# Kernel tuning notes

Measured on AMD Instinct MI355X. Metric: run time of the kernel, lower is better.

Reference implementation:

```python
import jax, jax.numpy as jnp
import numpy as np

B, W, KD, NC, D, NN, NH, AD, HOPS = 512, 4, 64, 32, 256, 16, 8, 32, 4
DH = D // NH
DFF = 4 * D
P = B * W + B
ROLE_WRITER, ROLE_QUERY = 0, 1


def setup_inputs() -> dict:
    key = jax.random.key(0)
    ks = iter(jax.random.split(key, 40))
    f = lambda shape, s=0.02: jax.random.normal(next(ks), shape, dtype=jnp.float32) * s
    inp = {
        'query_keys': jax.random.normal(next(ks), (B, KD), dtype=jnp.float32),
        'writer_keys': jax.random.normal(next(ks), (B, W, KD), dtype=jnp.float32),
        'key_proj_w': f((KD, D)), 'key_proj_b': jnp.zeros((D,), jnp.float32),
        'class_embed': f((NC, D)), 'role_embed': f((3, D)), 'start_node_embed': f((NN, D)),
        'input_ln_g': jnp.ones((D,), jnp.float32), 'input_ln_b': jnp.zeros((D,), jnp.float32),
        'ln1_g': jnp.ones((NN, D), jnp.float32), 'ln1_b': jnp.zeros((NN, D), jnp.float32),
        'wqkv': f((NN, D, 3 * D)), 'bqkv': jnp.zeros((NN, 3 * D), jnp.float32),
        'wo': f((NN, D, D)), 'bo': jnp.zeros((NN, D), jnp.float32),
        'ln2_g': jnp.ones((NN, D), jnp.float32), 'ln2_b': jnp.zeros((NN, D), jnp.float32),
        'w_fc1': f((NN, D, DFF)), 'b_fc1': jnp.zeros((NN, DFF), jnp.float32),
        'w_fc2': f((NN, DFF, D)), 'b_fc2': jnp.zeros((NN, D), jnp.float32),
        'delta_w': jnp.zeros((D, D), jnp.float32), 'delta_b': jnp.zeros((D,), jnp.float32),
        'dir_w': f((D, D)), 'dir_b': jnp.zeros((D,), jnp.float32),
        'mag_w': f((D, 1)), 'mag_b': jnp.full((1,), 2.5, jnp.float32),
        'out_w': f((D, NC)), 'out_b': jnp.zeros((NC,), jnp.float32),
        'address_table': jax.random.normal(next(ks), (NN, AD), dtype=jnp.float32),
        'query_start_nodes': jax.random.randint(next(ks), (B,), 0, NN),
        'writer_labels': jax.random.randint(next(ks), (B, W), 0, NC),
        'writer_start_nodes': jax.random.randint(next(ks), (B, W), 0, NN),
    }
    return inp


def _ln(x):
    m = jnp.mean(x, -1, keepdims=True)
    v = jnp.var(x, -1, keepdims=True)
    return (x - m) * jax.lax.rsqrt(v + 1e-5)


def _forward(query_keys, writer_keys, key_proj_w, key_proj_b, class_embed, role_embed,
             start_node_embed, input_ln_g, input_ln_b, ln1_g, ln1_b, wqkv, bqkv, wo, bo,
             ln2_g, ln2_b, w_fc1, b_fc1, w_fc2, b_fc2, delta_w, delta_b, dir_w, dir_b,
             mag_w, mag_b, out_w, out_b, address_table,
             query_start_nodes, writer_labels, writer_start_nodes):
    # ---- encode writers (encode_writers) ----
    fk = writer_keys.reshape(-1, KD)          # [B*W, KD]
    fl = writer_labels.reshape(-1)            # [B*W]
    fs = writer_start_nodes.reshape(-1)       # [B*W]
    learned_w = fk @ key_proj_w + key_proj_b + class_embed[fl] + start_node_embed[fs] + role_embed[ROLE_WRITER]
    sw = jnp.zeros_like(learned_w).at[:, :KD].set(fk)
    sw = sw.at[:, KD:KD + NC].set(jax.nn.one_hot(fl, NC, dtype=learned_w.dtype))
    enc_w = _ln(learned_w) * input_ln_g + input_ln_b + sw
    # ---- encode queries (encode_queries) ----
    learned_q = query_keys @ key_proj_w + key_proj_b + start_node_embed[query_start_nodes] + role_embed[ROLE_QUERY]
    sq = jnp.zeros_like(learned_q).at[:, :KD].set(query_keys)
    enc_q = _ln(learned_q) * input_ln_g + input_ln_b + sq

    h = jnp.concatenate([enc_w, enc_q], axis=0)          # [P, D]
    node = jnp.concatenate([fs, query_start_nodes], 0)   # [P] current compute node per packet

    inv_sqrt_dh = 1.0 / np.sqrt(DH).astype(np.float32)
    for _ in range(HOPS):
        oh = jax.nn.one_hot(node, NN, dtype=h.dtype)      # [P, NN] dispatch weights

        def pnl(x, Wn, bn):
            # per-node linear: gather-compute-scatter via MoE-style dense dispatch
            xe = jnp.einsum('pn,pd->npd', oh, x)          # [NN, P, din]
            ye = jnp.einsum('npd,ndf->npf', xe, Wn)       # [NN, P, dout]
            return jnp.einsum('npf,pn->pf', ye, oh) + oh @ bn

        # ComputeNodeCell: pre-LN attention among packets at the same node
        x = _ln(h) * (oh @ ln1_g) + oh @ ln1_b
        qkv = pnl(x, wqkv, bqkv)                          # [P, 3D]
        q, k, v = jnp.split(qkv, 3, axis=-1)
        q = q.reshape(P, NH, DH); k = k.reshape(P, NH, DH); v = v.reshape(P, NH, DH)
        scores = jnp.einsum('phd,qhd->hpq', q, k) * inv_sqrt_dh   # [NH, P, P]
        same = node[:, None] == node[None, :]
        scores = jnp.where(same[None], scores, -1e9)
        attn = jax.nn.softmax(scores, axis=-1)
        ao = jnp.einsum('hpq,qhd->phd', attn, v).reshape(P, D)
        h = h + pnl(ao, wo, bo)
        # MLP block
        x2 = _ln(h) * (oh @ ln2_g) + oh @ ln2_b
        h = h + pnl(jax.nn.gelu(pnl(x2, w_fc1, b_fc1)), w_fc2, b_fc2)
        # routing heads: pick next node from address table, apply gated delta
        direction = h @ dir_w + dir_b
        node = jnp.argmax(direction[:, :AD] @ address_table.T, axis=-1)
        h = h + (h @ delta_w + delta_b) * jax.nn.sigmoid(h @ mag_w + mag_b)

    return h @ out_w + out_b                              # [P, NC] per-packet logits


def reference(query_keys, writer_keys, key_proj_w, key_proj_b, class_embed, role_embed,
              start_node_embed, input_ln_g, input_ln_b, ln1_g, ln1_b, wqkv, bqkv, wo, bo,
              ln2_g, ln2_b, w_fc1, b_fc1, w_fc2, b_fc2, delta_w, delta_b, dir_w, dir_b,
              mag_w, mag_b, out_w, out_b, address_table,
              query_start_nodes, writer_labels, writer_start_nodes):
    return _forward(query_keys, writer_keys, key_proj_w, key_proj_b, class_embed, role_embed,
                    start_node_embed, input_ln_g, input_ln_b, ln1_g, ln1_b, wqkv, bqkv, wo, bo,
                    ln2_g, ln2_b, w_fc1, b_fc1, w_fc2, b_fc2, delta_w, delta_b, dir_w, dir_b,
                    mag_w, mag_b, out_w, out_b, address_table,
                    query_start_nodes, writer_labels, writer_start_nodes)
```

## Files before the change

kernel.cpp:

```cpp
#include <hip/hip_runtime.h>
#include <math.h>

#define B_    512
#define W_    4
#define KD_   64
#define NC_   32
#define D_    256
#define NN_   16
#define NH_   8
#define AD_   32
#define HOPS_ 4
#define DH_   32
#define DFF_  1024
#define P_    2560
#define BW_   2048
#define MAXT_ 56

#define INV_SQRT_DH 0.17677669529663687f

__device__ __forceinline__ float block_sum256(float v, float* red) {
#pragma unroll
  for (int off = 32; off > 0; off >>= 1) v += __shfl_xor(v, off, 64);
  int wid = threadIdx.x >> 6;
  if ((threadIdx.x & 63) == 0) red[wid] = v;
  __syncthreads();
  float s = red[0] + red[1] + red[2] + red[3];
  __syncthreads();
  return s;
}

__device__ __forceinline__ float gelu_tanh(float v) {
  float u = 0.7978845608028654f * (v + 0.044715f * v * v * v);
  return 0.5f * v * (1.0f + tanhf(u));
}

__global__ __launch_bounds__(256) void encode_kernel(
    const float* __restrict__ query_keys, const float* __restrict__ writer_keys,
    const float* __restrict__ kpw, const float* __restrict__ kpb,
    const float* __restrict__ ce, const float* __restrict__ re,
    const float* __restrict__ sne, const float* __restrict__ ilg,
    const float* __restrict__ ilb, const int* __restrict__ qsn,
    const int* __restrict__ wl, const int* __restrict__ wsn,
    float* __restrict__ h, int* __restrict__ node) {
  int p = blockIdx.x, t = threadIdx.x;
  __shared__ float fk[KD_];
  __shared__ float red[4];
  const float* key;
  int lab = -1, sn, role;
  if (p < BW_) { key = writer_keys + (size_t)p * KD_; lab = wl[p]; sn = wsn[p]; role = 0; }
  else { int b = p - BW_; key = query_keys + (size_t)b * KD_; sn = qsn[b]; role = 1; }
  if (t < KD_) fk[t] = key[t];
  __syncthreads();

  float acc = kpb[t] + sne[sn * D_ + t] + re[role * D_ + t];
  if (lab >= 0) acc += ce[lab * D_ + t];
#pragma unroll 8
  for (int i = 0; i < KD_; i++) acc += fk[i] * kpw[i * D_ + t];

  float mean = block_sum256(acc, red) * (1.0f / D_);
  float d = acc - mean;
  float var = block_sum256(d * d, red) * (1.0f / D_);
  float xn = d * (1.0f / sqrtf(var + 1e-5f));

  float sw = 0.0f;
  if (t < KD_) sw = fk[t];
  else if (lab >= 0 && t < KD_ + NC_) sw = (t - KD_ == lab) ? 1.0f : 0.0f;

  h[(size_t)p * D_ + t] = xn * ilg[t] + ilb[t] + sw;
  if (t == 0) node[p] = sn;
}

__global__ __launch_bounds__(256) void sort_kernel(const int* __restrict__ node,
                                                   int* __restrict__ order,
                                                   int* __restrict__ invord,
                                                   int* __restrict__ offs,
                                                   int* __restrict__ cnts,
                                                   int* __restrict__ tnode,
                                                   int* __restrict__ tstart,
                                                   int* __restrict__ tend,
                                                   int* __restrict__ ntiles) {
  __shared__ int c[NN_], o[NN_], cur[NN_];
  int t = threadIdx.x;
  if (t < NN_) c[t] = 0;
  __syncthreads();
  for (int p = t; p < P_; p += 256) atomicAdd(&c[node[p]], 1);
  __syncthreads();
  if (t == 0) {
    int s = 0;
    for (int n = 0; n < NN_; n++) { o[n] = s; cur[n] = s; s += c[n]; }
    int idx = 0;
    for (int n = 0; n < NN_; n++) {
      int e = o[n] + c[n];
      for (int m0 = o[n]; m0 < e; m0 += 64) {
        tnode[idx] = n; tstart[idx] = m0; tend[idx] = e; idx++;
      }
    }
    ntiles[0] = idx;
  }
  __syncthreads();
  if (t < NN_) { cnts[t] = c[t]; offs[t] = o[t]; }
  for (int p = t; p < P_; p += 256) {
    int r = atomicAdd(&cur[node[p]], 1);
    order[r] = p;
    invord[p] = r;
  }
}

__global__ __launch_bounds__(256) void ln_affine(const float* __restrict__ h,
                                                 const float* __restrict__ g,
                                                 const float* __restrict__ b,
                                                 const int* __restrict__ node,
                                                 const int* __restrict__ order,
                                                 float* __restrict__ x) {
  int sp = blockIdx.x * 4 + (threadIdx.x >> 6);
  int lane = threadIdx.x & 63;
  int p = order[sp];
  int n = node[p];
  float4 v = *(const float4*)&h[(size_t)p * D_ + lane * 4];
  float s = v.x + v.y + v.z + v.w;
#pragma unroll
  for (int off = 32; off > 0; off >>= 1) s += __shfl_xor(s, off, 64);
  float mean = s * (1.0f / D_);
  float4 d = make_float4(v.x - mean, v.y - mean, v.z - mean, v.w - mean);
  float vr = d.x * d.x + d.y * d.y + d.z * d.z + d.w * d.w;
#pragma unroll
  for (int off = 32; off > 0; off >>= 1) vr += __shfl_xor(vr, off, 64);
  float inv = 1.0f / sqrtf(vr * (1.0f / D_) + 1e-5f);
  float4 gg = *(const float4*)&g[n * D_ + lane * 4];
  float4 bb = *(const float4*)&b[n * D_ + lane * 4];
  float4 o;
  o.x = d.x * inv * gg.x + bb.x;
  o.y = d.y * inv * gg.y + bb.y;
  o.z = d.z * inv * gg.z + bb.z;
  o.w = d.w * inv * gg.w + bb.w;
  *(float4*)&x[(size_t)sp * D_ + lane * 4] = o;
}

template <int DIN, int DOUT, int JT, int ACT, int RESID, int PER_NODE, int KSPLIT, int XMODE>
__global__ __launch_bounds__(256) void glin(const float* __restrict__ x,
                                            const float* __restrict__ W,
                                            const float* __restrict__ bias,
                                            float* __restrict__ out,
                                            float* __restrict__ pbuf,
                                            const float* __restrict__ xaux,
                                            const int* __restrict__ order,
                                            const int* __restrict__ invord,
                                            const int* __restrict__ tnode,
                                            const int* __restrict__ tstart,
                                            const int* __restrict__ tend,
                                            const int* __restrict__ ntiles) {
  constexpr int KC = 32, STX = 68;
  constexpr int CPT = JT / 16;
  constexpr int HALF = 64;
  constexpr int KLEN = DIN / KSPLIT;
  constexpr int NCH = KLEN / KC;
  constexpr int LPR = JT / 4;
  constexpr int RPI = 64 / LPR;

  int ti = blockIdx.x;
  int n, s0, s1;
  if (PER_NODE) {
    if (ti >= ntiles[0]) return;
    n = tnode[ti]; s0 = tstart[ti]; s1 = tend[ti];
  } else {
    n = 0; s0 = ti * 64; s1 = P_;
  }
  int jbase = blockIdx.y * JT;
  int kz = (KSPLIT > 1) ? blockIdx.z : 0;
  int k0 = kz * KLEN;
  int rows = s1 - s0; if (rows > 64) rows = 64;

  __shared__ float xs[2][KC][STX];
  __shared__ float ws[2][KC][JT];

  int tid = threadIdx.x;
  const float* Wn = W + (size_t)n * DIN * DOUT + jbase;

  int xrow = tid >> 2, xq = tid & 3;
  bool xvalid = xrow < rows;
  const float* xptr = x + (size_t)(s0 + (xvalid ? xrow : 0)) * DIN + k0 + xq * 4;
  const float* aptr = nullptr;
  if (XMODE == 1) {
    int pr = xvalid ? invord[s0 + xrow] : 0;
    aptr = xaux + (size_t)pr * DIN + k0 + xq * 4;
  }

  float4 xr0, xr1;
  auto xfetch = [&](int kc) {
    if (xvalid) {
      xr0 = *(const float4*)(xptr + kc);
      xr1 = *(const float4*)(xptr + kc + 16);
      if (XMODE == 1) {
        float4 p0 = *(const float4*)(aptr + kc);
        float4 p1 = *(const float4*)(aptr + kc + 16);
        xr0.x += p0.x; xr0.y += p0.y; xr0.z += p0.z; xr0.w += p0.w;
        xr1.x += p1.x; xr1.y += p1.y; xr1.z += p1.z; xr1.w += p1.w;
      }
    } else {
      xr0 = make_float4(0.f, 0.f, 0.f, 0.f);
      xr1 = make_float4(0.f, 0.f, 0.f, 0.f);
    }
  };
  auto xstage = [&](int buf) {
    xs[buf][xq * 4 + 0][xrow] = xr0.x;
    xs[buf][xq * 4 + 1][xrow] = xr0.y;
    xs[buf][xq * 4 + 2][xrow] = xr0.z;
    xs[buf][xq * 4 + 3][xrow] = xr0.w;
    xs[buf][xq * 4 + 16][xrow] = xr1.x;
    xs[buf][xq * 4 + 17][xrow] = xr1.y;
    xs[buf][xq * 4 + 18][xrow] = xr1.z;
    xs[buf][xq * 4 + 19][xrow] = xr1.w;
  };
  int wvw = tid >> 6, lane = tid & 63;
  int wlr = lane / LPR;
  int wlc = (lane % LPR) * 4;
  auto wfetch = [&](int buf, int kc) {
#pragma unroll
    for (int i = 0; i < 8 / RPI; i++) {
      int kr = wvw * 8 + i * RPI;
      const float* g = &Wn[(size_t)(k0 + kc + kr + wlr) * DOUT + wlc];
      __builtin_amdgcn_global_load_lds(
          (const __attribute__((address_space(1))) unsigned int*)g,
          (__attribute__((address_space(3))) unsigned int*)&ws[buf][kr][0],
          16, 0, 0);
    }
  };

  wfetch(0, 0);
  xfetch(0);
  xstage(0);
  __syncthreads();

  int r4 = (tid >> 4) * 4;
  int jc4 = (tid & 15) * 4;
  float acc[4][CPT];
#pragma unroll
  for (int r = 0; r < 4; r++)
#pragma unroll
    for (int cc = 0; cc < CPT; cc++) acc[r][cc] = 0.f;

  for (int c = 0; c < NCH; c++) {
    int cur = c & 1;
    if (c + 1 < NCH) {
      wfetch(cur ^ 1, (c + 1) * KC);
      xfetch((c + 1) * KC);
    }
#pragma unroll 8
    for (int k = 0; k < KC; k++) {
      float4 a = *(const float4*)&xs[cur][k][r4];
      float av[4] = {a.x, a.y, a.z, a.w};
      float bv[CPT];
      float4 b0 = *(const float4*)&ws[cur][k][jc4];
      bv[0] = b0.x; bv[1] = b0.y; bv[2] = b0.z; bv[3] = b0.w;
      if (CPT == 8) {
        float4 b1 = *(const float4*)&ws[cur][k][jc4 + HALF];
        bv[4] = b1.x; bv[5] = b1.y; bv[6] = b1.z; bv[7] = b1.w;
      }
#pragma unroll
      for (int r = 0; r < 4; r++)
#pragma unroll
        for (int cc = 0; cc < CPT; cc++) acc[r][cc] += av[r] * bv[cc];
    }
    if (c + 1 < NCH) xstage(cur ^ 1);
    __syncthreads();
  }

  bool main_part = (KSPLIT == 1) || (kz == 0);
  float bbv[CPT];
#pragma unroll
  for (int cc = 0; cc < 4; cc++) bbv[cc] = bias[n * DOUT + jbase + jc4 + cc];
  if (CPT == 8) {
#pragma unroll
    for (int cc = 0; cc < 4; cc++) bbv[4 + cc] = bias[n * DOUT + jbase + jc4 + HALF + cc];
  }

#pragma unroll
  for (int r = 0; r < 4; r++) {
    int lr = r4 + r;
    if (lr >= rows) continue;
    float v[CPT];
    if (main_part) {
#pragma unroll
      for (int cc = 0; cc < CPT; cc++) {
        v[cc] = acc[r][cc] + bbv[cc];
        if (ACT == 1) v[cc] = gelu_tanh(v[cc]);
      }
      if (RESID) {
        int pp = PER_NODE ? order[s0 + lr] : (s0 + lr);
        float* op = &out[(size_t)pp * DOUT + jbase + jc4];
        {
          float4 old = *(const float4*)op;
          *(float4*)op = make_float4(v[0] + old.x, v[1] + old.y, v[2] + old.z, v[3] + old.w);
        }
        if (CPT == 8) {
          float4 old = *(const float4*)(op + HALF);
          *(float4*)(op + HALF) =
              make_float4(v[4] + old.x, v[5] + old.y, v[6] + old.z, v[7] + old.w);
        }
      } else {
        float* op = &out[(size_t)(s0 + lr) * DOUT + jbase + jc4];
        *(float4*)op = make_float4(v[0], v[1], v[2], v[3]);
        if (CPT == 8)
          *(float4*)(op + HALF) = make_float4(v[4], v[5], v[6], v[7]);
      }
    } else {
      float* op = &pbuf[(size_t)(s0 + lr) * DOUT + jbase + jc4];
      *(float4*)op = make_float4(acc[r][0], acc[r][1], acc[r][2], acc[r][3]);
      if (CPT == 8)
        *(float4*)(op + HALF) = make_float4(acc[r][4], acc[r][5], acc[r][6], acc[r][7]);
    }
  }
}

#define ATS 36
__global__ __launch_bounds__(256) void attn_kernel(const float* __restrict__ qkv,
                                                   const int* __restrict__ node,
                                                   const int* __restrict__ order,
                                                   const int* __restrict__ offs,
                                                   const int* __restrict__ cnts,
                                                   float* __restrict__ ao) {
  __shared__ float qs[32 * ATS];
  __shared__ float kts[32 * ATS];
  __shared__ float vs[32 * ATS];
  __shared__ float ps[32 * ATS];
  __shared__ int glo[32], ghi[32];

  int t = threadIdx.x;
  int r = t >> 3;
  int j4 = (t & 7) * 4;
  int r0 = blockIdx.x * 32;
  int hd = blockIdx.y;

  if (t < 32) {
    int n = node[order[r0 + t]];
    glo[t] = offs[n];
    ghi[t] = offs[n] + cnts[n];
  }
  __syncthreads();

  {
    const float* qp = &qkv[(size_t)(r0 + r) * 768 + hd * 32 + j4];
    float4 q4 = *(const float4*)qp;
    q4.x *= INV_SQRT_DH; q4.y *= INV_SQRT_DH; q4.z *= INV_SQRT_DH; q4.w *= INV_SQRT_DH;
    *(float4*)&qs[r * ATS + j4] = q4;
  }

  int lo = glo[0];
  int hi = ghi[31];
  int myglo = glo[r], myghi = ghi[r];

  float4 o4 = {0.f, 0.f, 0.f, 0.f};
  float mrow = -1e30f, lrow = 0.f;

  for (int kt = lo; kt < hi; kt += 32) {
    int sj = kt + r;
    float4 k4 = {0.f, 0.f, 0.f, 0.f}, v4 = {0.f, 0.f, 0.f, 0.f};
    if (sj < hi) {
      const float* kp = &qkv[(size_t)sj * 768 + 256 + hd * 32 + j4];
      k4 = *(const float4*)kp;
      v4 = *(const float4*)(kp + 256);
    }
    __syncthreads();
    kts[(j4 + 0) * ATS + r] = k4.x;
    kts[(j4 + 1) * ATS + r] = k4.y;
    kts[(j4 + 2) * ATS + r] = k4.z;
    kts[(j4 + 3) * ATS + r] = k4.w;
    *(float4*)&vs[r * ATS + j4] = v4;
    __syncthreads();

    float s0 = 0.f, s1 = 0.f, s2 = 0.f, s3 = 0.f;
#pragma unroll 8
    for (int d = 0; d < 32; d++) {
      float qv = qs[r * ATS + d];
      float4 kv = *(const float4*)&kts[d * ATS + j4];
      s0 += qv * kv.x; s1 += qv * kv.y; s2 += qv * kv.z; s3 += qv * kv.w;
    }
    int c0 = kt + j4;
    if (c0 + 0 < myglo || c0 + 0 >= myghi) s0 = -1e30f;
    if (c0 + 1 < myglo || c0 + 1 >= myghi) s1 = -1e30f;
    if (c0 + 2 < myglo || c0 + 2 >= myghi) s2 = -1e30f;
    if (c0 + 3 < myglo || c0 + 3 >= myghi) s3 = -1e30f;

    float mx = fmaxf(fmaxf(s0, s1), fmaxf(s2, s3));
#pragma unroll
    for (int off = 4; off > 0; off >>= 1) mx = fmaxf(mx, __shfl_xor(mx, off, 8));
    float mnew = fmaxf(mrow, mx);
    float alpha = __expf(mrow - mnew);
    float p0 = __expf(s0 - mnew), p1 = __expf(s1 - mnew);
    float p2 = __expf(s2 - mnew), p3 = __expf(s3 - mnew);
    float ls = p0 + p1 + p2 + p3;
#pragma unroll
    for (int off = 4; off > 0; off >>= 1) ls += __shfl_xor(ls, off, 8);
    lrow = lrow * alpha + ls;
    mrow = mnew;
    o4.x *= alpha; o4.y *= alpha; o4.z *= alpha; o4.w *= alpha;

    *(float4*)&ps[r * ATS + j4] = make_float4(p0, p1, p2, p3);
#pragma unroll 8
    for (int j = 0; j < 32; j++) {
      float pj = ps[r * ATS + j];
      float4 vv = *(const float4*)&vs[j * ATS + j4];
      o4.x += pj * vv.x; o4.y += pj * vv.y; o4.z += pj * vv.z; o4.w += pj * vv.w;
    }
  }

  float inv = 1.f / lrow;
  o4.x *= inv; o4.y *= inv; o4.z *= inv; o4.w *= inv;
  *(float4*)&ao[(size_t)(r0 + r) * D_ + hd * 32 + j4] = o4;
}

__global__ __launch_bounds__(256) void route_kernel(float* __restrict__ h,
                                                    const float* __restrict__ pbuf,
                                                    const int* __restrict__ invord,
                                                    const float* __restrict__ dir_w,
                                                    const float* __restrict__ dir_b,
                                                    const float* __restrict__ at,
                                                    const float* __restrict__ mag_w,
                                                    const float* __restrict__ mag_b,
                                                    const float* __restrict__ delta,
                                                    int* __restrict__ node) {
  int p = blockIdx.x, t = threadIdx.x;
  __shared__ float hs[D_];
  __shared__ float dpart[8][AD_];
  __shared__ float dirs[AD_];
  __shared__ float scs[NN_];
  __shared__ float red[4];
  float hv = h[(size_t)p * D_ + t] + pbuf[(size_t)invord[p] * D_ + t];
  hs[t] = hv;
  __syncthreads();

  int j = t & 31, seg = t >> 5;
  float part = 0.0f;
#pragma unroll 8
  for (int i = 0; i < 32; i++) {
    int ii = seg * 32 + i;
    part += hs[ii] * dir_w[ii * D_ + j];
  }
  dpart[seg][j] = part;
  __syncthreads();
  if (t < AD_) {
    float s = dir_b[t];
#pragma unroll
    for (int g = 0; g < 8; g++) s += dpart[g][t];
    dirs[t] = s;
  }
  __syncthreads();
  if (t < NN_) {
    float s = 0.0f;
#pragma unroll
    for (int a = 0; a < AD_; a++) s += dirs[a] * at[t * AD_ + a];
    scs[t] = s;
  }
  __syncthreads();
  if (t == 0) {
    float best = scs[0];
    int arg = 0;
    for (int nn = 1; nn < NN_; nn++)
      if (scs[nn] > best) { best = scs[nn]; arg = nn; }
    node[p] = arg;
  }
  float mag = block_sum256(hv * mag_w[t], red) + mag_b[0];
  float sig = 1.0f / (1.0f + __expf(-mag));
  h[(size_t)p * D_ + t] = hv + delta[(size_t)p * D_ + t] * sig;
}

__global__ __launch_bounds__(256) void out_kernel(const float* __restrict__ h,
                                                  const float* __restrict__ ow,
                                                  const float* __restrict__ ob,
                                                  float* __restrict__ out) {
  int p = blockIdx.x, t = threadIdx.x;
  __shared__ float hs[D_];
  __shared__ float part[8][NC_];
  hs[t] = h[(size_t)p * D_ + t];
  __syncthreads();
  int j = t & 31, seg = t >> 5;
  float s = 0.0f;
#pragma unroll 8
  for (int i = 0; i < 32; i++) {
    int ii = seg * 32 + i;
    s += hs[ii] * ow[ii * NC_ + j];
  }
  part[seg][j] = s;
  __syncthreads();
  if (t < NC_) {
    float r = ob[t];
#pragma unroll
    for (int g = 0; g < 8; g++) r += part[g][t];
    out[(size_t)p * NC_ + t] = r;
  }
}

extern "C" void kernel_launch(void* const* d_in, const int* in_sizes, int n_in,
                              void* d_out, int out_size, void* d_ws, size_t ws_size,
                              hipStream_t stream) {
  (void)in_sizes; (void)n_in; (void)out_size; (void)ws_size;
  const float* query_keys       = (const float*)d_in[0];
  const float* writer_keys      = (const float*)d_in[1];
  const float* key_proj_w       = (const float*)d_in[2];
  const float* key_proj_b       = (const float*)d_in[3];
  const float* class_embed      = (const float*)d_in[4];
  const float* role_embed       = (const float*)d_in[5];
  const float* start_node_embed = (const float*)d_in[6];
  const float* input_ln_g       = (const float*)d_in[7];
  const float* input_ln_b       = (const float*)d_in[8];
  const float* ln1_g            = (const float*)d_in[9];
  const float* ln1_b            = (const float*)d_in[10];
  const float* wqkv             = (const float*)d_in[11];
  const float* bqkv             = (const float*)d_in[12];
  const float* wo               = (const float*)d_in[13];
  const float* bo               = (const float*)d_in[14];
  const float* ln2_g            = (const float*)d_in[15];
  const float* ln2_b            = (const float*)d_in[16];
  const float* w_fc1            = (const float*)d_in[17];
  const float* b_fc1            = (const float*)d_in[18];
  const float* w_fc2            = (const float*)d_in[19];
  const float* b_fc2            = (const float*)d_in[20];
  const float* delta_w          = (const float*)d_in[21];
  const float* delta_b          = (const float*)d_in[22];
  const float* dir_w            = (const float*)d_in[23];
  const float* dir_b            = (const float*)d_in[24];
  const float* mag_w            = (const float*)d_in[25];
  const float* mag_b            = (const float*)d_in[26];
  const float* out_w            = (const float*)d_in[27];
  const float* out_b            = (const float*)d_in[28];
  const float* address_table    = (const float*)d_in[29];
  const int* query_start_nodes  = (const int*)d_in[30];
  const int* writer_labels      = (const int*)d_in[31];
  const int* writer_start_nodes = (const int*)d_in[32];

  uintptr_t basep = (uintptr_t)d_ws;
  auto carve = [&](size_t bytes) {
    basep = (basep + 255) & ~(uintptr_t)255;
    void* r = (void*)basep;
    basep += bytes;
    return r;
  };
  float* h    = (float*)carve((size_t)P_ * D_ * 4);
  float* x    = (float*)carve((size_t)P_ * D_ * 4);
  float* buf1 = (float*)carve((size_t)P_ * DFF_ * 4);
  float* ff   = (float*)carve((size_t)P_ * DFF_ * 4);
  float* pbuf = (float*)carve((size_t)P_ * D_ * 4);
  int* node   = (int*)carve(P_ * 4);
  int* order  = (int*)carve(P_ * 4);
  int* invord = (int*)carve(P_ * 4);
  int* offs   = (int*)carve(NN_ * 4);
  int* cnts   = (int*)carve(NN_ * 4);
  int* tnode  = (int*)carve(MAXT_ * 4);
  int* tstart = (int*)carve(MAXT_ * 4);
  int* tend   = (int*)carve(MAXT_ * 4);
  int* ntiles = (int*)carve(4);

  encode_kernel<<<P_, 256, 0, stream>>>(query_keys, writer_keys, key_proj_w, key_proj_b,
                                        class_embed, role_embed, start_node_embed,
                                        input_ln_g, input_ln_b, query_start_nodes,
                                        writer_labels, writer_start_nodes, h, node);

  for (int hop = 0; hop < HOPS_; ++hop) {
    sort_kernel<<<1, 256, 0, stream>>>(node, order, invord, offs, cnts,
                                       tnode, tstart, tend, ntiles);
    ln_affine<<<P_ / 4, 256, 0, stream>>>(h, ln1_g, ln1_b, node, order, x);
    glin<256, 768, 64, 0, 0, 1, 1, 0><<<dim3(MAXT_, 12), 256, 0, stream>>>(
        x, wqkv, bqkv, buf1, nullptr, nullptr, order, invord, tnode, tstart, tend,
        ntiles);
    attn_kernel<<<dim3(P_ / 32, NH_), 256, 0, stream>>>(buf1, node, order, offs,
                                                        cnts, x );
    glin<256, 256, 64, 0, 1, 1, 1, 0><<<dim3(MAXT_, 4), 256, 0, stream>>>(
        x, wo, bo, h, nullptr, nullptr, order, invord, tnode, tstart, tend, ntiles);
    ln_affine<<<P_ / 4, 256, 0, stream>>>(h, ln2_g, ln2_b, node, order, x);
    glin<256, 1024, 64, 1, 0, 1, 1, 0><<<dim3(MAXT_, 16), 256, 0, stream>>>(
        x, w_fc1, b_fc1, ff, nullptr, nullptr, order, invord, tnode, tstart, tend,
        ntiles);
    glin<1024, 256, 64, 0, 1, 1, 2, 0><<<dim3(MAXT_, 4, 2), 256, 0, stream>>>(
        ff, w_fc2, b_fc2, h, pbuf, nullptr, order, invord, tnode, tstart, tend,
        ntiles);
    glin<256, 256, 64, 0, 0, 0, 1, 1><<<dim3(P_ / 64, 4), 256, 0, stream>>>(
        h, delta_w, delta_b, buf1 , nullptr, pbuf, order, invord,
        tnode, tstart, tend, ntiles);
    route_kernel<<<P_, 256, 0, stream>>>(h, pbuf, invord, dir_w, dir_b, address_table,
                                         mag_w, mag_b, buf1, node);
  }

  out_kernel<<<P_, 256, 0, stream>>>(h, out_w, out_b, (float*)d_out);
}
```

Baseline: 910.1 us.

## Replace LDS-tiled grouped GEMM with register-streamed 16-row tiles and XCD swizzle

Replaces the shared-memory double-buffered GEMM with a kernel that streams weights straight from global memory into registers. Each wave handles 4 rows of a 16-row tile and each thread owns 4 output columns across a 256-wide column block. The sort kernel now emits 16-row tiles per node, which cuts padding waste for small node groups. Block indices are also swizzled across XCDs. In exchange, each weight is reused by fewer rows, so weight traffic through L2 rises, and activation buffers are padded so tail tiles can read past the last row safely.

```diff
diff --git a/kernel.cpp b/kernel.cpp
--- a/kernel.cpp
+++ b/kernel.cpp
@@ -14,7 +14,7 @@
 #define DFF_  1024
 #define P_    2560
 #define BW_   2048
-#define MAXT_ 56
+#define MAXT2_ 176
 
 #define INV_SQRT_DH 0.17677669529663687f
 
@@ -91,7 +91,7 @@
     int idx = 0;
     for (int n = 0; n < NN_; n++) {
       int e = o[n] + c[n];
-      for (int m0 = o[n]; m0 < e; m0 += 64) {
+      for (int m0 = o[n]; m0 < e; m0 += 16) {
         tnode[idx] = n; tstart[idx] = m0; tend[idx] = e; idx++;
       }
     }
@@ -136,178 +136,151 @@
   *(float4*)&x[(size_t)sp * D_ + lane * 4] = o;
 }
 
-template <int DIN, int DOUT, int JT, int ACT, int RESID, int PER_NODE, int KSPLIT, int XMODE>
-__global__ __launch_bounds__(256) void glin(const float* __restrict__ x,
-                                            const float* __restrict__ W,
-                                            const float* __restrict__ bias,
-                                            float* __restrict__ out,
-                                            float* __restrict__ pbuf,
-                                            const float* __restrict__ xaux,
-                                            const int* __restrict__ order,
-                                            const int* __restrict__ invord,
-                                            const int* __restrict__ tnode,
-                                            const int* __restrict__ tstart,
-                                            const int* __restrict__ tend,
-                                            const int* __restrict__ ntiles) {
-  constexpr int KC = 32, STX = 68;
-  constexpr int CPT = JT / 16;
-  constexpr int HALF = 64;
+template <int DIN, int DOUT, int ACT, int RESID, int PER_NODE, int KSPLIT, int XMODE>
+__global__ __launch_bounds__(256) void glin2(const float* __restrict__ x,
+                                             const float* __restrict__ W,
+                                             const float* __restrict__ bias,
+                                             float* __restrict__ out,
+                                             float* __restrict__ pbuf,
+                                             const float* __restrict__ xaux,
+                                             const int* __restrict__ order,
+                                             const int* __restrict__ invord,
+                                             const int* __restrict__ tnode,
+                                             const int* __restrict__ tstart,
+                                             const int* __restrict__ tend,
+                                             const int* __restrict__ ntiles) {
   constexpr int KLEN = DIN / KSPLIT;
-  constexpr int NCH = KLEN / KC;
-  constexpr int LPR = JT / 4;
-  constexpr int RPI = 64 / LPR;
-
-  int ti = blockIdx.x;
-  int n, s0, s1;
+
+  int gx = gridDim.x;
+  int bid = blockIdx.x;
+  int ti = (bid & 7) * (gx >> 3) + (bid >> 3);
+
+  int n, s0, rows;
   if (PER_NODE) {
     if (ti >= ntiles[0]) return;
-    n = tnode[ti]; s0 = tstart[ti]; s1 = tend[ti];
+    n = tnode[ti];
+    s0 = tstart[ti];
+    int e = tend[ti];
+    rows = e - s0;
+    if (rows > 16) rows = 16;
   } else {
-    n = 0; s0 = ti * 64; s1 = P_;
-  }
-  int jbase = blockIdx.y * JT;
+    n = 0;
+    s0 = ti * 16;
+    rows = 16;
+  }
+  int jb = blockIdx.y * 256;
   int kz = (KSPLIT > 1) ? blockIdx.z : 0;
   int k0 = kz * KLEN;
-  int rows = s1 - s0; if (rows > 64) rows = 64;
-
-  __shared__ float xs[2][KC][STX];
-  __shared__ float ws[2][KC][JT];
 
   int tid = threadIdx.x;
-  const float* Wn = W + (size_t)n * DIN * DOUT + jbase;
-
-  int xrow = tid >> 2, xq = tid & 3;
-  bool xvalid = xrow < rows;
-  const float* xptr = x + (size_t)(s0 + (xvalid ? xrow : 0)) * DIN + k0 + xq * 4;
-  const float* aptr = nullptr;
-  if (XMODE == 1) {
-    int pr = xvalid ? invord[s0 + xrow] : 0;
-    aptr = xaux + (size_t)pr * DIN + k0 + xq * 4;
-  }
-
-  float4 xr0, xr1;
-  auto xfetch = [&](int kc) {
-    if (xvalid) {
-      xr0 = *(const float4*)(xptr + kc);
-      xr1 = *(const float4*)(xptr + kc + 16);
-      if (XMODE == 1) {
-        float4 p0 = *(const float4*)(aptr + kc);
-        float4 p1 = *(const float4*)(aptr + kc + 16);
-        xr0.x += p0.x; xr0.y += p0.y; xr0.z += p0.z; xr0.w += p0.w;
-        xr1.x += p1.x; xr1.y += p1.y; xr1.z += p1.z; xr1.w += p1.w;
-      }
-    } else {
-      xr0 = make_float4(0.f, 0.f, 0.f, 0.f);
-      xr1 = make_float4(0.f, 0.f, 0.f, 0.f);
-    }
-  };
-  auto xstage = [&](int buf) {
-    xs[buf][xq * 4 + 0][xrow] = xr0.x;
-    xs[buf][xq * 4 + 1][xrow] = xr0.y;
-    xs[buf][xq * 4 + 2][xrow] = xr0.z;
-    xs[buf][xq * 4 + 3][xrow] = xr0.w;
-    xs[buf][xq * 4 + 16][xrow] = xr1.x;
-    xs[buf][xq * 4 + 17][xrow] = xr1.y;
-    xs[buf][xq * 4 + 18][xrow] = xr1.z;
-    xs[buf][xq * 4 + 19][xrow] = xr1.w;
-  };
-  int wvw = tid >> 6, lane = tid & 63;
-  int wlr = lane / LPR;
-  int wlc = (lane % LPR) * 4;
-  auto wfetch = [&](int buf, int kc) {
-#pragma unroll
-    for (int i = 0; i < 8 / RPI; i++) {
-      int kr = wvw * 8 + i * RPI;
-      const float* g = &Wn[(size_t)(k0 + kc + kr + wlr) * DOUT + wlc];
-      __builtin_amdgcn_global_load_lds(
-          (const __attribute__((address_space(1))) unsigned int*)g,
-          (__attribute__((address_space(3))) unsigned int*)&ws[buf][kr][0],
-          16, 0, 0);
-    }
-  };
-
-  wfetch(0, 0);
-  xfetch(0);
-  xstage(0);
-  __syncthreads();
-
-  int r4 = (tid >> 4) * 4;
-  int jc4 = (tid & 15) * 4;
-  float acc[4][CPT];
-#pragma unroll
-  for (int r = 0; r < 4; r++)
-#pragma unroll
-    for (int cc = 0; cc < CPT; cc++) acc[r][cc] = 0.f;
-
-  for (int c = 0; c < NCH; c++) {
-    int cur = c & 1;
-    if (c + 1 < NCH) {
-      wfetch(cur ^ 1, (c + 1) * KC);
-      xfetch((c + 1) * KC);
-    }
-#pragma unroll 8
-    for (int k = 0; k < KC; k++) {
-      float4 a = *(const float4*)&xs[cur][k][r4];
-      float av[4] = {a.x, a.y, a.z, a.w};
-      float bv[CPT];
-      float4 b0 = *(const float4*)&ws[cur][k][jc4];
-      bv[0] = b0.x; bv[1] = b0.y; bv[2] = b0.z; bv[3] = b0.w;
-      if (CPT == 8) {
-        float4 b1 = *(const float4*)&ws[cur][k][jc4 + HALF];
-        bv[4] = b1.x; bv[5] = b1.y; bv[6] = b1.z; bv[7] = b1.w;
-      }
-#pragma unroll
-      for (int r = 0; r < 4; r++)
-#pragma unroll
-        for (int cc = 0; cc < CPT; cc++) acc[r][cc] += av[r] * bv[cc];
-    }
-    if (c + 1 < NCH) xstage(cur ^ 1);
-    __syncthreads();
-  }
-
+  int wv = __builtin_amdgcn_readfirstlane((int)(tid >> 6));
+  int j4 = (tid & 63) << 2;
+
+  const float* Wp = W + (size_t)n * DIN * DOUT + (size_t)k0 * DOUT + jb + j4;
+
+  const float* xr0;
+  const float* xr1;
+  const float* xr2;
+  const float* xr3;
+  const float* ar0 = nullptr;
+  const float* ar1 = nullptr;
+  const float* ar2 = nullptr;
+  const float* ar3 = nullptr;
+  {
+    int rbase = s0 + (wv << 2);
+    xr0 = x + (size_t)(rbase + 0) * DIN + k0;
+    xr1 = x + (size_t)(rbase + 1) * DIN + k0;
+    xr2 = x + (size_t)(rbase + 2) * DIN + k0;
+    xr3 = x + (size_t)(rbase + 3) * DIN + k0;
+    if (XMODE == 1) {
+      ar0 = xaux + (size_t)invord[rbase + 0] * DIN + k0;
+      ar1 = xaux + (size_t)invord[rbase + 1] * DIN + k0;
+      ar2 = xaux + (size_t)invord[rbase + 2] * DIN + k0;
+      ar3 = xaux + (size_t)invord[rbase + 3] * DIN + k0;
+    }
+  }
+
+  float4 a0 = make_float4(0.f, 0.f, 0.f, 0.f);
+  float4 a1 = a0, a2 = a0, a3 = a0;
+  float4 wc0, wc1, wc2, wc3, xc0, xc1, xc2, xc3;
+
+#define LDW_(kk, w0, w1, w2, w3)                              \
+  w0 = *(const float4*)(Wp + (size_t)((kk) + 0) * DOUT);      \
+  w1 = *(const float4*)(Wp + (size_t)((kk) + 1) * DOUT);      \
+  w2 = *(const float4*)(Wp + (size_t)((kk) + 2) * DOUT);      \
+  w3 = *(const float4*)(Wp + (size_t)((kk) + 3) * DOUT);
+
+#define LDX1_(kk, ptr, aptr, dst)                             \
+  dst = *(const float4*)((ptr) + (kk));                       \
+  if (XMODE == 1) {                                           \
+    float4 _a = *(const float4*)((aptr) + (kk));              \
+    dst.x += _a.x; dst.y += _a.y; dst.z += _a.z; dst.w += _a.w; \
+  }
+
+#define LDX_(kk, x0, x1, x2, x3)   \
+  LDX1_(kk, xr0, ar0, x0)          \
+  LDX1_(kk, xr1, ar1, x1)          \
+  LDX1_(kk, xr2, ar2, x2)          \
+  LDX1_(kk, xr3, ar3, x3)
+
+  LDW_(0, wc0, wc1, wc2, wc3);
+  LDX_(0, xc0, xc1, xc2, xc3);
+
+#pragma unroll 2
+  for (int kk = 0; kk < KLEN; kk += 4) {
+    float4 wn0, wn1, wn2, wn3, xn0, xn1, xn2, xn3;
+    bool more = (kk + 4 < KLEN);
+    if (more) {
+      LDW_(kk + 4, wn0, wn1, wn2, wn3);
+      LDX_(kk + 4, xn0, xn1, xn2, xn3);
+    }
+#pragma unroll
+    for (int t = 0; t < 4; ++t) {
+      float4 wt = (t == 0) ? wc0 : (t == 1) ? wc1 : (t == 2) ? wc2 : wc3;
+      float f0 = (t == 0) ? xc0.x : (t == 1) ? xc0.y : (t == 2) ? xc0.z : xc0.w;
+      float f1 = (t == 0) ? xc1.x : (t == 1) ? xc1.y : (t == 2) ? xc1.z : xc1.w;
+      float f2 = (t == 0) ? xc2.x : (t == 1) ? xc2.y : (t == 2) ? xc2.z : xc2.w;
+      float f3 = (t == 0) ? xc3.x : (t == 1) ? xc3.y : (t == 2) ? xc3.z : xc3.w;
+      a0.x += f0 * wt.x; a0.y += f0 * wt.y; a0.z += f0 * wt.z; a0.w += f0 * wt.w;
+      a1.x += f1 * wt.x; a1.y += f1 * wt.y; a1.z += f1 * wt.z; a1.w += f1 * wt.w;
+      a2.x += f2 * wt.x; a2.y += f2 * wt.y; a2.z += f2 * wt.z; a2.w += f2 * wt.w;
+      a3.x += f3 * wt.x; a3.y += f3 * wt.y; a3.z += f3 * wt.z; a3.w += f3 * wt.w;
+    }
+    if (more) {
+      wc0 = wn0; wc1 = wn1; wc2 = wn2; wc3 = wn3;
+      xc0 = xn0; xc1 = xn1; xc2 = xn2; xc3 = xn3;
+    }
+  }
+#undef LDW_
+#undef LDX1_
+#undef LDX_
+
+  int jcol = jb + j4;
   bool main_part = (KSPLIT == 1) || (kz == 0);
-  float bbv[CPT];
-#pragma unroll
-  for (int cc = 0; cc < 4; cc++) bbv[cc] = bias[n * DOUT + jbase + jc4 + cc];
-  if (CPT == 8) {
-#pragma unroll
-    for (int cc = 0; cc < 4; cc++) bbv[4 + cc] = bias[n * DOUT + jbase + jc4 + HALF + cc];
-  }
-
-#pragma unroll
-  for (int r = 0; r < 4; r++) {
-    int lr = r4 + r;
-    if (lr >= rows) continue;
-    float v[CPT];
+  float4 bv = make_float4(0.f, 0.f, 0.f, 0.f);
+  if (main_part) bv = *(const float4*)(bias + (size_t)n * DOUT + jcol);
+
+#pragma unroll
+  for (int r = 0; r < 4; ++r) {
+    int lr = (wv << 2) + r;
+    if (PER_NODE && lr >= rows) continue;
+    float4 av = (r == 0) ? a0 : (r == 1) ? a1 : (r == 2) ? a2 : a3;
     if (main_part) {
-#pragma unroll
-      for (int cc = 0; cc < CPT; cc++) {
-        v[cc] = acc[r][cc] + bbv[cc];
-        if (ACT == 1) v[cc] = gelu_tanh(v[cc]);
+      float4 v = make_float4(av.x + bv.x, av.y + bv.y, av.z + bv.z, av.w + bv.w);
+      if (ACT == 1) {
+        v.x = gelu_tanh(v.x); v.y = gelu_tanh(v.y);
+        v.z = gelu_tanh(v.z); v.w = gelu_tanh(v.w);
       }
       if (RESID) {
         int pp = PER_NODE ? order[s0 + lr] : (s0 + lr);
-        float* op = &out[(size_t)pp * DOUT + jbase + jc4];
-        {
-          float4 old = *(const float4*)op;
-          *(float4*)op = make_float4(v[0] + old.x, v[1] + old.y, v[2] + old.z, v[3] + old.w);
-        }
-        if (CPT == 8) {
-          float4 old = *(const float4*)(op + HALF);
-          *(float4*)(op + HALF) =
-              make_float4(v[4] + old.x, v[5] + old.y, v[6] + old.z, v[7] + old.w);
-        }
+        float* op = out + (size_t)pp * DOUT + jcol;
+        float4 old = *(const float4*)op;
+        *(float4*)op = make_float4(v.x + old.x, v.y + old.y, v.z + old.z, v.w + old.w);
       } else {
-        float* op = &out[(size_t)(s0 + lr) * DOUT + jbase + jc4];
-        *(float4*)op = make_float4(v[0], v[1], v[2], v[3]);
-        if (CPT == 8)
-          *(float4*)(op + HALF) = make_float4(v[4], v[5], v[6], v[7]);
+        *(float4*)(out + (size_t)(s0 + lr) * DOUT + jcol) = v;
       }
     } else {
-      float* op = &pbuf[(size_t)(s0 + lr) * DOUT + jbase + jc4];
-      *(float4*)op = make_float4(acc[r][0], acc[r][1], acc[r][2], acc[r][3]);
-      if (CPT == 8)
-        *(float4*)(op + HALF) = make_float4(acc[r][4], acc[r][5], acc[r][6], acc[r][7]);
+      *(float4*)(pbuf + (size_t)(s0 + lr) * DOUT + jcol) = av;
     }
   }
 }
@@ -535,19 +508,19 @@
     basep += bytes;
     return r;
   };
-  float* h    = (float*)carve((size_t)P_ * D_ * 4);
-  float* x    = (float*)carve((size_t)P_ * D_ * 4);
-  float* buf1 = (float*)carve((size_t)P_ * DFF_ * 4);
-  float* ff   = (float*)carve((size_t)P_ * DFF_ * 4);
-  float* pbuf = (float*)carve((size_t)P_ * D_ * 4);
+  float* h    = (float*)carve((size_t)(P_ + 16) * D_ * 4);
+  float* x    = (float*)carve((size_t)(P_ + 16) * D_ * 4);
+  float* buf1 = (float*)carve((size_t)(P_ + 16) * DFF_ * 4);
+  float* ff   = (float*)carve((size_t)(P_ + 16) * DFF_ * 4);
+  float* pbuf = (float*)carve((size_t)(P_ + 16) * D_ * 4);
   int* node   = (int*)carve(P_ * 4);
   int* order  = (int*)carve(P_ * 4);
   int* invord = (int*)carve(P_ * 4);
   int* offs   = (int*)carve(NN_ * 4);
   int* cnts   = (int*)carve(NN_ * 4);
-  int* tnode  = (int*)carve(MAXT_ * 4);
-  int* tstart = (int*)carve(MAXT_ * 4);
-  int* tend   = (int*)carve(MAXT_ * 4);
+  int* tnode  = (int*)carve(MAXT2_ * 4);
+  int* tstart = (int*)carve(MAXT2_ * 4);
+  int* tend   = (int*)carve(MAXT2_ * 4);
   int* ntiles = (int*)carve(4);
 
   encode_kernel<<<P_, 256, 0, stream>>>(query_keys, writer_keys, key_proj_w, key_proj_b,
@@ -559,21 +532,21 @@
     sort_kernel<<<1, 256, 0, stream>>>(node, order, invord, offs, cnts,
                                        tnode, tstart, tend, ntiles);
     ln_affine<<<P_ / 4, 256, 0, stream>>>(h, ln1_g, ln1_b, node, order, x);
-    glin<256, 768, 64, 0, 0, 1, 1, 0><<<dim3(MAXT_, 12), 256, 0, stream>>>(
+    glin2<256, 768, 0, 0, 1, 1, 0><<<dim3(MAXT2_, 3), 256, 0, stream>>>(
         x, wqkv, bqkv, buf1, nullptr, nullptr, order, invord, tnode, tstart, tend,
         ntiles);
     attn_kernel<<<dim3(P_ / 32, NH_), 256, 0, stream>>>(buf1, node, order, offs,
                                                         cnts, x );
-    glin<256, 256, 64, 0, 1, 1, 1, 0><<<dim3(MAXT_, 4), 256, 0, stream>>>(
+    glin2<256, 256, 0, 1, 1, 1, 0><<<dim3(MAXT2_, 1), 256, 0, stream>>>(
         x, wo, bo, h, nullptr, nullptr, order, invord, tnode, tstart, tend, ntiles);
     ln_affine<<<P_ / 4, 256, 0, stream>>>(h, ln2_g, ln2_b, node, order, x);
-    glin<256, 1024, 64, 1, 0, 1, 1, 0><<<dim3(MAXT_, 16), 256, 0, stream>>>(
+    glin2<256, 1024, 1, 0, 1, 1, 0><<<dim3(MAXT2_, 4), 256, 0, stream>>>(
         x, w_fc1, b_fc1, ff, nullptr, nullptr, order, invord, tnode, tstart, tend,
         ntiles);
-    glin<1024, 256, 64, 0, 1, 1, 2, 0><<<dim3(MAXT_, 4, 2), 256, 0, stream>>>(
+    glin2<1024, 256, 0, 1, 1, 2, 0><<<dim3(MAXT2_, 1, 2), 256, 0, stream>>>(
         ff, w_fc2, b_fc2, h, pbuf, nullptr, order, invord, tnode, tstart, tend,
         ntiles);
-    glin<256, 256, 64, 0, 0, 0, 1, 1><<<dim3(P_ / 64, 4), 256, 0, stream>>>(
+    glin2<256, 256, 0, 0, 0, 1, 1><<<dim3(P_ / 16, 1), 256, 0, stream>>>(
         h, delta_w, delta_b, buf1 , nullptr, pbuf, order, invord,
         tnode, tstart, tend, ntiles);
     route_kernel<<<P_, 256, 0, stream>>>(h, pbuf, invord, dir_w, dir_b, address_table,
```

Result: slower. 1.079 ms (+18.5%).

## Use split-bf16 MFMA for per-node QKV and FFN GEMMs with transposed weight prep

Applied to the files above, without the earlier changes.

Replaces the fp32 tiled GEMMs for the QKV, FC1 and FC2 projections with MFMA 16x16x32 bf16 kernels. These use a three-term hi/lo bf16 split to keep close to fp32 accuracy. Weights are transposed and split once per call, activations are written as hi/lo bf16 by the layernorm and FC1 epilogues, and tiles shrink to 16 rows. FC2 no longer uses the K-split partial buffer and adds its residual directly into h, so the route kernel no longer folds in pbuf. The cost is extra weight-prep kernels and triple MFMA work, in exchange for matrix-core throughput.

```diff
diff --git a/kernel.cpp b/kernel.cpp
--- a/kernel.cpp
+++ b/kernel.cpp
@@ -14,9 +14,26 @@
 #define DFF_  1024
 #define P_    2560
 #define BW_   2048
-#define MAXT_ 56
+#define MAXT_  56
+#define MAXT2_ 176
+#define PS_   (P_ + 16)
 
 #define INV_SQRT_DH 0.17677669529663687f
+
+typedef __attribute__((ext_vector_type(8))) short short8v;
+typedef __attribute__((ext_vector_type(4))) float f32x4;
+
+__device__ __forceinline__ unsigned short bf16_rne(float f) {
+  unsigned u = __float_as_uint(f);
+  unsigned r = (u + 0x7fffu + ((u >> 16) & 1u)) >> 16;
+  return (unsigned short)r;
+}
+__device__ __forceinline__ void split2(float v, unsigned short& h, unsigned short& l) {
+  unsigned short hb = bf16_rne(v);
+  float hf = __uint_as_float(((unsigned)hb) << 16);
+  h = hb;
+  l = bf16_rne(v - hf);
+}
 
 __device__ __forceinline__ float block_sum256(float v, float* red) {
 #pragma unroll
@@ -32,6 +49,21 @@
 __device__ __forceinline__ float gelu_tanh(float v) {
   float u = 0.7978845608028654f * (v + 0.044715f * v * v * v);
   return 0.5f * v * (1.0f + tanhf(u));
+}
+
+__global__ __launch_bounds__(256) void padzero_kernel(unsigned short* __restrict__ xh,
+                                                      unsigned short* __restrict__ xl,
+                                                      unsigned short* __restrict__ ffh,
+                                                      unsigned short* __restrict__ ffl) {
+  int t = threadIdx.x;
+  for (int i = t; i < 16 * D_; i += 256) {
+    xh[(size_t)P_ * D_ + i] = 0;
+    xl[(size_t)P_ * D_ + i] = 0;
+  }
+  for (int i = t; i < 16 * DFF_; i += 256) {
+    ffh[(size_t)P_ * DFF_ + i] = 0;
+    ffl[(size_t)P_ * DFF_ + i] = 0;
+  }
 }
 
 __global__ __launch_bounds__(256) void encode_kernel(
@@ -75,10 +107,14 @@
                                                    int* __restrict__ invord,
                                                    int* __restrict__ offs,
                                                    int* __restrict__ cnts,
-                                                   int* __restrict__ tnode,
-                                                   int* __restrict__ tstart,
-                                                   int* __restrict__ tend,
-                                                   int* __restrict__ ntiles) {
+                                                   int* __restrict__ tnode64,
+                                                   int* __restrict__ tstart64,
+                                                   int* __restrict__ tend64,
+                                                   int* __restrict__ ntiles64,
+                                                   int* __restrict__ tnode16,
+                                                   int* __restrict__ tstart16,
+                                                   int* __restrict__ tend16,
+                                                   int* __restrict__ ntiles16) {
   __shared__ int c[NN_], o[NN_], cur[NN_];
   int t = threadIdx.x;
   if (t < NN_) c[t] = 0;
@@ -88,14 +124,18 @@
   if (t == 0) {
     int s = 0;
     for (int n = 0; n < NN_; n++) { o[n] = s; cur[n] = s; s += c[n]; }
-    int idx = 0;
+    int i64 = 0, i16 = 0;
     for (int n = 0; n < NN_; n++) {
       int e = o[n] + c[n];
       for (int m0 = o[n]; m0 < e; m0 += 64) {
-        tnode[idx] = n; tstart[idx] = m0; tend[idx] = e; idx++;
+        tnode64[i64] = n; tstart64[i64] = m0; tend64[i64] = e; i64++;
       }
-    }
-    ntiles[0] = idx;
+      for (int m0 = o[n]; m0 < e; m0 += 16) {
+        tnode16[i16] = n; tstart16[i16] = m0; tend16[i16] = e; i16++;
+      }
+    }
+    ntiles64[0] = i64;
+    ntiles16[0] = i16;
   }
   __syncthreads();
   if (t < NN_) { cnts[t] = c[t]; offs[t] = o[t]; }
@@ -111,7 +151,8 @@
                                                  const float* __restrict__ b,
                                                  const int* __restrict__ node,
                                                  const int* __restrict__ order,
-                                                 float* __restrict__ x) {
+                                                 unsigned short* __restrict__ xh,
+                                                 unsigned short* __restrict__ xl) {
   int sp = blockIdx.x * 4 + (threadIdx.x >> 6);
   int lane = threadIdx.x & 63;
   int p = order[sp];
@@ -128,12 +169,109 @@
   float inv = 1.0f / sqrtf(vr * (1.0f / D_) + 1e-5f);
   float4 gg = *(const float4*)&g[n * D_ + lane * 4];
   float4 bb = *(const float4*)&b[n * D_ + lane * 4];
-  float4 o;
-  o.x = d.x * inv * gg.x + bb.x;
-  o.y = d.y * inv * gg.y + bb.y;
-  o.z = d.z * inv * gg.z + bb.z;
-  o.w = d.w * inv * gg.w + bb.w;
-  *(float4*)&x[(size_t)sp * D_ + lane * 4] = o;
+  float o[4];
+  o[0] = d.x * inv * gg.x + bb.x;
+  o[1] = d.y * inv * gg.y + bb.y;
+  o[2] = d.z * inv * gg.z + bb.z;
+  o[3] = d.w * inv * gg.w + bb.w;
+  ushort4 oh, ol;
+  split2(o[0], oh.x, ol.x);
+  split2(o[1], oh.y, ol.y);
+  split2(o[2], oh.z, ol.z);
+  split2(o[3], oh.w, ol.w);
+  *(ushort4*)&xh[(size_t)sp * D_ + lane * 4] = oh;
+  *(ushort4*)&xl[(size_t)sp * D_ + lane * 4] = ol;
+}
+
+template <int K, int C>
+__global__ __launch_bounds__(256) void wprep(const float* __restrict__ W,
+                                             unsigned short* __restrict__ th,
+                                             unsigned short* __restrict__ tl) {
+  __shared__ float ld[32][33];
+  int n = blockIdx.z;
+  int k0 = blockIdx.x * 32, c0 = blockIdx.y * 32;
+  int tx = threadIdx.x & 31, ty = threadIdx.x >> 5;
+  const float* Wn = W + (size_t)n * K * C;
+#pragma unroll
+  for (int i = 0; i < 32; i += 8)
+    ld[i + ty][tx] = Wn[(size_t)(k0 + i + ty) * C + c0 + tx];
+  __syncthreads();
+#pragma unroll
+  for (int i = 0; i < 32; i += 8) {
+    float v = ld[tx][i + ty];
+    unsigned short hh, ll;
+    split2(v, hh, ll);
+    size_t off = ((size_t)n * C + c0 + i + ty) * K + k0 + tx;
+    th[off] = hh;
+    tl[off] = ll;
+  }
+}
+
+template <int DIN, int DOUT, int ACT, int RESID, int SPLITOUT>
+__global__ __launch_bounds__(256) void gmfma(
+    const unsigned short* __restrict__ xh, const unsigned short* __restrict__ xl,
+    const unsigned short* __restrict__ wth, const unsigned short* __restrict__ wtl,
+    const float* __restrict__ bias, float* __restrict__ outf,
+    unsigned short* __restrict__ outh, unsigned short* __restrict__ outl,
+    const int* __restrict__ order, const int* __restrict__ tnode,
+    const int* __restrict__ tstart, const int* __restrict__ tend,
+    const int* __restrict__ ntiles) {
+  int gx = gridDim.x;
+  int bid = blockIdx.x;
+  int ti = (bid & 7) * (gx >> 3) + (bid >> 3);
+  if (ti >= ntiles[0]) return;
+  int n = tnode[ti];
+  int s0 = tstart[ti];
+  int rows = tend[ti] - s0;
+  if (rows <= 0) return;
+  if (rows > 16) rows = 16;
+
+  int tid = threadIdx.x;
+  int wv = tid >> 6;
+  int lane = tid & 63;
+  int r16 = lane & 15;
+  int kg = lane >> 4;
+  int jcol = blockIdx.y * 64 + wv * 16;
+
+  const unsigned short* pah = xh + (size_t)(s0 + r16) * DIN + kg * 8;
+  const unsigned short* pal = xl + (size_t)(s0 + r16) * DIN + kg * 8;
+  const unsigned short* pbh = wth + ((size_t)n * DOUT + jcol + r16) * DIN + kg * 8;
+  const unsigned short* pbl = wtl + ((size_t)n * DOUT + jcol + r16) * DIN + kg * 8;
+
+  f32x4 acc0 = {0.f, 0.f, 0.f, 0.f};
+  f32x4 acc1 = acc0, acc2 = acc0;
+#pragma unroll 4
+  for (int k0 = 0; k0 < DIN; k0 += 32) {
+    short8v ah = *(const short8v*)(pah + k0);
+    short8v al = *(const short8v*)(pal + k0);
+    short8v bh = *(const short8v*)(pbh + k0);
+    short8v bl = *(const short8v*)(pbl + k0);
+    acc0 = __builtin_amdgcn_mfma_f32_16x16x32_bf16(ah, bh, acc0, 0, 0, 0);
+    acc1 = __builtin_amdgcn_mfma_f32_16x16x32_bf16(ah, bl, acc1, 0, 0, 0);
+    acc2 = __builtin_amdgcn_mfma_f32_16x16x32_bf16(al, bh, acc2, 0, 0, 0);
+  }
+
+  float bv = bias[(size_t)n * DOUT + jcol + r16];
+#pragma unroll
+  for (int rg = 0; rg < 4; rg++) {
+    int r = kg * 4 + rg;
+    if (r >= rows) continue;
+    float v = acc0[rg] + acc1[rg] + acc2[rg] + bv;
+    if (ACT) v = gelu_tanh(v);
+    if (SPLITOUT) {
+      size_t off = (size_t)(s0 + r) * DOUT + jcol + r16;
+      unsigned short hh, ll;
+      split2(v, hh, ll);
+      outh[off] = hh;
+      outl[off] = ll;
+    } else if (RESID) {
+      int pp = order[s0 + r];
+      float* op = outf + (size_t)pp * DOUT + jcol + r16;
+      *op += v;
+    } else {
+      outf[(size_t)(s0 + r) * DOUT + jcol + r16] = v;
+    }
+  }
 }
 
 template <int DIN, int DOUT, int JT, int ACT, int RESID, int PER_NODE, int KSPLIT, int XMODE>
@@ -410,8 +548,6 @@
 }
 
 __global__ __launch_bounds__(256) void route_kernel(float* __restrict__ h,
-                                                    const float* __restrict__ pbuf,
-                                                    const int* __restrict__ invord,
                                                     const float* __restrict__ dir_w,
                                                     const float* __restrict__ dir_b,
                                                     const float* __restrict__ at,
@@ -425,7 +561,7 @@
   __shared__ float dirs[AD_];
   __shared__ float scs[NN_];
   __shared__ float red[4];
-  float hv = h[(size_t)p * D_ + t] + pbuf[(size_t)invord[p] * D_ + t];
+  float hv = h[(size_t)p * D_ + t];
   hs[t] = hv;
   __syncthreads();
 
@@ -537,18 +673,35 @@
   };
   float* h    = (float*)carve((size_t)P_ * D_ * 4);
   float* x    = (float*)carve((size_t)P_ * D_ * 4);
-  float* buf1 = (float*)carve((size_t)P_ * DFF_ * 4);
-  float* ff   = (float*)carve((size_t)P_ * DFF_ * 4);
-  float* pbuf = (float*)carve((size_t)P_ * D_ * 4);
+  float* buf1 = (float*)carve((size_t)P_ * 768 * 4);
+  unsigned short* xh  = (unsigned short*)carve((size_t)PS_ * D_ * 2);
+  unsigned short* xl  = (unsigned short*)carve((size_t)PS_ * D_ * 2);
+  unsigned short* ffh = (unsigned short*)carve((size_t)PS_ * DFF_ * 2);
+  unsigned short* ffl = (unsigned short*)carve((size_t)PS_ * DFF_ * 2);
+  unsigned short* wtqh = (unsigned short*)carve((size_t)NN_ * 768 * 256 * 2);
+  unsigned short* wtql = (unsigned short*)carve((size_t)NN_ * 768 * 256 * 2);
+  unsigned short* wt1h = (unsigned short*)carve((size_t)NN_ * 1024 * 256 * 2);
+  unsigned short* wt1l = (unsigned short*)carve((size_t)NN_ * 1024 * 256 * 2);
+  unsigned short* wt2h = (unsigned short*)carve((size_t)NN_ * 256 * 1024 * 2);
+  unsigned short* wt2l = (unsigned short*)carve((size_t)NN_ * 256 * 1024 * 2);
   int* node   = (int*)carve(P_ * 4);
   int* order  = (int*)carve(P_ * 4);
   int* invord = (int*)carve(P_ * 4);
   int* offs   = (int*)carve(NN_ * 4);
   int* cnts   = (int*)carve(NN_ * 4);
-  int* tnode  = (int*)carve(MAXT_ * 4);
-  int* tstart = (int*)carve(MAXT_ * 4);
-  int* tend   = (int*)carve(MAXT_ * 4);
-  int* ntiles = (int*)carve(4);
+  int* tnode64  = (int*)carve(MAXT_ * 4);
+  int* tstart64 = (int*)carve(MAXT_ * 4);
+  int* tend64   = (int*)carve(MAXT_ * 4);
+  int* ntiles64 = (int*)carve(4);
+  int* tnode16  = (int*)carve(MAXT2_ * 4);
+  int* tstart16 = (int*)carve(MAXT2_ * 4);
+  int* tend16   = (int*)carve(MAXT2_ * 4);
+  int* ntiles16 = (int*)carve(4);
+
+  padzero_kernel<<<1, 256, 0, stream>>>(xh, xl, ffh, ffl);
+  wprep<256, 768><<<dim3(8, 24, NN_), 256, 0, stream>>>(wqkv, wtqh, wtql);
+  wprep<256, 1024><<<dim3(8, 32, NN_), 256, 0, stream>>>(w_fc1, wt1h, wt1l);
+  wprep<1024, 256><<<dim3(32, 8, NN_), 256, 0, stream>>>(w_fc2, wt2h, wt2l);
 
   encode_kernel<<<P_, 256, 0, stream>>>(query_keys, writer_keys, key_proj_w, key_proj_b,
                                         class_embed, role_embed, start_node_embed,
@@ -557,26 +710,28 @@
 
   for (int hop = 0; hop < HOPS_; ++hop) {
     sort_kernel<<<1, 256, 0, stream>>>(node, order, invord, offs, cnts,
-                                       tnode, tstart, tend, ntiles);
-    ln_affine<<<P_ / 4, 256, 0, stream>>>(h, ln1_g, ln1_b, node, order, x);
-    glin<256, 768, 64, 0, 0, 1, 1, 0><<<dim3(MAXT_, 12), 256, 0, stream>>>(
-        x, wqkv, bqkv, buf1, nullptr, nullptr, order, invord, tnode, tstart, tend,
-        ntiles);
+                                       tnode64, tstart64, tend64, ntiles64,
+                                       tnode16, tstart16, tend16, ntiles16);
+    ln_affine<<<P_ / 4, 256, 0, stream>>>(h, ln1_g, ln1_b, node, order, xh, xl);
+    gmfma<256, 768, 0, 0, 0><<<dim3(MAXT2_, 12), 256, 0, stream>>>(
+        xh, xl, wtqh, wtql, bqkv, buf1, nullptr, nullptr, order,
+        tnode16, tstart16, tend16, ntiles16);
     attn_kernel<<<dim3(P_ / 32, NH_), 256, 0, stream>>>(buf1, node, order, offs,
                                                         cnts, x );
     glin<256, 256, 64, 0, 1, 1, 1, 0><<<dim3(MAXT_, 4), 256, 0, stream>>>(
-        x, wo, bo, h, nullptr, nullptr, order, invord, tnode, tstart, tend, ntiles);
-    ln_affine<<<P_ / 4, 256, 0, stream>>>(h, ln2_g, ln2_b, node, order, x);
-    glin<256, 1024, 64, 1, 0, 1, 1, 0><<<dim3(MAXT_, 16), 256, 0, stream>>>(
-        x, w_fc1, b_fc1, ff, nullptr, nullptr, order, invord, tnode, tstart, tend,
-        ntiles);
-    glin<1024, 256, 64, 0, 1, 1, 2, 0><<<dim3(MAXT_, 4, 2), 256, 0, stream>>>(
-        ff, w_fc2, b_fc2, h, pbuf, nullptr, order, invord, tnode, tstart, tend,
-        ntiles);
-    glin<256, 256, 64, 0, 0, 0, 1, 1><<<dim3(P_ / 64, 4), 256, 0, stream>>>(
-        h, delta_w, delta_b, buf1 , nullptr, pbuf, order, invord,
-        tnode, tstart, tend, ntiles);
-    route_kernel<<<P_, 256, 0, stream>>>(h, pbuf, invord, dir_w, dir_b, address_table,
+        x, wo, bo, h, nullptr, nullptr, order, invord, tnode64, tstart64, tend64,
+        ntiles64);
+    ln_affine<<<P_ / 4, 256, 0, stream>>>(h, ln2_g, ln2_b, node, order, xh, xl);
+    gmfma<256, 1024, 1, 0, 1><<<dim3(MAXT2_, 16), 256, 0, stream>>>(
+        xh, xl, wt1h, wt1l, b_fc1, nullptr, ffh, ffl, order,
+        tnode16, tstart16, tend16, ntiles16);
+    gmfma<1024, 256, 0, 1, 0><<<dim3(MAXT2_, 4), 256, 0, stream>>>(
+        ffh, ffl, wt2h, wt2l, b_fc2, h, nullptr, nullptr, order,
+        tnode16, tstart16, tend16, ntiles16);
+    glin<256, 256, 64, 0, 0, 0, 1, 0><<<dim3(P_ / 64, 4), 256, 0, stream>>>(
+        h, delta_w, delta_b, buf1 , nullptr, nullptr, order, invord,
+        tnode64, tstart64, tend64, ntiles64);
+    route_kernel<<<P_, 256, 0, stream>>>(h, dir_w, dir_b, address_table,
                                          mag_w, mag_b, buf1, node);
   }
 
```

Measured after the change: 1.072 ms. 1.18x slower.
